# Kernel optimization log

Measured on AMD Instinct MI355X. Metric: run time of the kernel, lower is better.

Reference implementation:

```python
import jax, jax.numpy as jnp
import numpy as np

RC = 5.0
ATOM_TYPES = jnp.array([1, 6, 7, 8], dtype=jnp.int64)
L = 40.0   # cubic box edge; rc <= 0.5*L so the MIC branch of the torch module applies
N = 6000


def setup_inputs() -> dict:
    key = jax.random.key(0)
    k1, k2 = jax.random.split(key)
    coord = jax.random.uniform(k1, (N, 3), dtype=jnp.float32) * L
    cell = jnp.eye(3, dtype=jnp.float32) * L
    elems = jnp.array([1, 6, 7, 8])[jax.random.randint(k2, (N,), 0, 4)]
    return {"coord": coord, "cell": cell, "elems": elems}


def reference(coord, cell, elems):
    """JAX equivalent of PreprocessLayerTorch (MIC branch, rc <= min cell length / 2).

    The torch module emits a dynamic list of directed pairs ind_2 plus integer
    shifts; under jit we return the fixed-shape dense equivalent:
      - onehot:      (n, n_types) bool, AtomicOnehot of elems
      - dist_masked: (n, n) float, |r_j - r_i|_MIC where 0 < d < rc, else 0
      - shift:       (n, n, 3) int32 MIC lattice shifts
    ind_2 == nonzero(dist_masked > 0); same math, fixed shapes.
    """
    onehot = elems[:, None] == ATOM_TYPES[None, :]            # (n, n_types)

    h_inv = jnp.linalg.inv(cell)
    frac = coord @ h_inv                                      # (n, 3) fractional
    frac = frac - jnp.floor(frac)                             # wrap into [0,1)

    # dfrac[i, j] = frac_j - frac_i, minimum-image convention
    dfrac = frac[None, :, :] - frac[:, None, :]               # (n, n, 3)
    shift = -jnp.round(dfrac)                                 # (n, n, 3)
    dfrac = dfrac + shift
    d = dfrac @ cell                                          # (n, n, 3) Cartesian
    dist2 = jnp.sum(d * d, axis=-1)                           # (n, n)

    mask = (dist2 > 0.0) & (dist2 < RC * RC)
    dist = jnp.sqrt(jnp.where(mask, dist2, 1.0))              # safe sqrt
    dist_masked = jnp.where(mask, dist, 0.0)
    return onehot, dist_masked, shift.astype(jnp.int32)
```

## Files before the change

### kernel.cpp

```cpp
#include <hip/hip_runtime.h>
#include <math.h>

#define RC2 25.0f

typedef float f32x4 __attribute__((ext_vector_type(4)));

__global__ __launch_bounds__(256) void prep_kernel(
    const float* __restrict__ coord,
    const float* __restrict__ cell,
    const int* __restrict__ elems,
    float* __restrict__ onehot,
    float* __restrict__ frac,
    int n)
{
    int i = blockIdx.x * blockDim.x + threadIdx.x;
    if (i >= n) return;

    float a = cell[0], b = cell[1], c = cell[2];
    float d = cell[3], e = cell[4], f = cell[5];
    float g = cell[6], h = cell[7], k = cell[8];
    float A =  (e * k - f * h);
    float B = -(d * k - f * g);
    float C =  (d * h - e * g);
    float det = a * A + b * B + c * C;
    float inv = 1.0f / det;
    float m00 = A * inv,              m01 = -(b * k - c * h) * inv, m02 =  (b * f - c * e) * inv;
    float m10 = B * inv,              m11 =  (a * k - c * g) * inv, m12 = -(a * f - c * d) * inv;
    float m20 = C * inv,              m21 = -(a * h - b * g) * inv, m22 =  (a * e - b * d) * inv;

    float x = coord[i * 3 + 0];
    float y = coord[i * 3 + 1];
    float z = coord[i * 3 + 2];
    float fx = x * m00 + y * m10 + z * m20;
    float fy = x * m01 + y * m11 + z * m21;
    float fz = x * m02 + y * m12 + z * m22;
    fx -= floorf(fx); fy -= floorf(fy); fz -= floorf(fz);
    frac[i * 3 + 0] = fx;
    frac[i * 3 + 1] = fy;
    frac[i * 3 + 2] = fz;

    int el = elems[i];
    f32x4 oh;
    oh.x = (el == 1) ? 1.0f : 0.0f;
    oh.y = (el == 6) ? 1.0f : 0.0f;
    oh.z = (el == 7) ? 1.0f : 0.0f;
    oh.w = (el == 8) ? 1.0f : 0.0f;
    __builtin_nontemporal_store(oh, (f32x4*)(onehot + (size_t)i * 4));
}

__global__ __launch_bounds__(256) void pair_kernel(
    const float* __restrict__ frac,
    const float* __restrict__ cell,
    float* __restrict__ dist,
    float* __restrict__ shift,
    int n)
{
    __shared__ float sh_lds[1024 * 3];

    const int i  = blockIdx.y;
    const int J0 = blockIdx.x * 1024;
    const int t  = threadIdx.x;
    const int j0 = J0 + t * 4;

    if (j0 < n) {
        float c00 = cell[0], c01 = cell[1], c02 = cell[2];
        float c10 = cell[3], c11 = cell[4], c12 = cell[5];
        float c20 = cell[6], c21 = cell[7], c22 = cell[8];

        float fi0 = frac[i * 3 + 0];
        float fi1 = frac[i * 3 + 1];
        float fi2 = frac[i * 3 + 2];

        const float4* fj4 = (const float4*)(frac + (size_t)j0 * 3);
        float4 va = fj4[0], vb = fj4[1], vc = fj4[2];
        float fj[4][3] = {
            {va.x, va.y, va.z},
            {va.w, vb.x, vb.y},
            {vb.z, vb.w, vc.x},
            {vc.y, vc.z, vc.w}
        };

        f32x4 dout;
        float4 sh[3];
        float* shf = (float*)sh;

#pragma unroll
        for (int q = 0; q < 4; q++) {
            float d0 = fj[q][0] - fi0;
            float d1 = fj[q][1] - fi1;
            float d2 = fj[q][2] - fi2;
            float s0 = -rintf(d0);
            float s1 = -rintf(d1);
            float s2 = -rintf(d2);
            d0 += s0; d1 += s1; d2 += s2;
            float x = d0 * c00 + d1 * c10 + d2 * c20;
            float y = d0 * c01 + d1 * c11 + d2 * c21;
            float z = d0 * c02 + d1 * c12 + d2 * c22;
            float r2 = x * x + y * y + z * z;
            bool m = (r2 > 0.0f) && (r2 < RC2);
            dout[q] = m ? sqrtf(r2) : 0.0f;
            shf[q * 3 + 0] = s0;
            shf[q * 3 + 1] = s1;
            shf[q * 3 + 2] = s2;
        }

        __builtin_nontemporal_store(dout, (f32x4*)(dist + (size_t)i * n + j0));

        float4* lp = (float4*)(sh_lds + t * 12);
        lp[0] = sh[0];
        lp[1] = sh[1];
        lp[2] = sh[2];
    }

    __syncthreads();

    const int len = min(1024, n - J0);
    const int nf4 = (len * 3) >> 2;
    const f32x4* ls = (const f32x4*)sh_lds;
    f32x4* gp = (f32x4*)(shift + ((size_t)i * n + J0) * 3);
#pragma unroll
    for (int k = 0; k < 3; k++) {
        int q = k * 256 + t;
        if (q < nf4) __builtin_nontemporal_store(ls[q], gp + q);
    }
}

extern "C" void kernel_launch(void* const* d_in, const int* in_sizes, int n_in,
                              void* d_out, int out_size, void* d_ws, size_t ws_size,
                              hipStream_t stream)
{
    const float* coord = (const float*)d_in[0];
    const float* cell  = (const float*)d_in[1];
    const int*   elems = (const int*)d_in[2];
    int n = in_sizes[2];

    float* out    = (float*)d_out;
    float* onehot = out;
    float* dist   = out + (size_t)n * 4;
    float* shift  = out + (size_t)n * 4 + (size_t)n * n;

    float* frac = (float*)d_ws;

    dim3 b1(256);
    dim3 g1((n + 255) / 256);
    prep_kernel<<<g1, b1, 0, stream>>>(coord, cell, elems, onehot, frac, n);

    dim3 b2(256);
    dim3 g2((n + 1023) / 1024, n);
    pair_kernel<<<g2, b2, 0, stream>>>(frac, cell, dist, shift, n);
}
```

Baseline: 558.2 us.

## Use persistent grid-stride blocks and store shifts directly without LDS staging

```diff
diff --git a/kernel.cpp b/kernel.cpp
--- a/kernel.cpp
+++ b/kernel.cpp
@@ -53,19 +53,19 @@
     const float* __restrict__ cell,
     float* __restrict__ dist,
     float* __restrict__ shift,
-    int n)
+    int n, int nchunk, int total)
 {
-    __shared__ float sh_lds[1024 * 3];
+    const int t = threadIdx.x;
 
-    const int i  = blockIdx.y;
-    const int J0 = blockIdx.x * 1024;
-    const int t  = threadIdx.x;
-    const int j0 = J0 + t * 4;
+    float c00 = cell[0], c01 = cell[1], c02 = cell[2];
+    float c10 = cell[3], c11 = cell[4], c12 = cell[5];
+    float c20 = cell[6], c21 = cell[7], c22 = cell[8];
 
-    if (j0 < n) {
-        float c00 = cell[0], c01 = cell[1], c02 = cell[2];
-        float c10 = cell[3], c11 = cell[4], c12 = cell[5];
-        float c20 = cell[6], c21 = cell[7], c22 = cell[8];
+    for (int chunk = blockIdx.x; chunk < total; chunk += gridDim.x) {
+        int i  = chunk / nchunk;
+        int c  = chunk - i * nchunk;
+        int j0 = c * 1024 + t * 4;
+        if (j0 >= n) continue;
 
         float fi0 = frac[i * 3 + 0];
         float fi1 = frac[i * 3 + 1];
@@ -81,7 +81,7 @@
         };
 
         f32x4 dout;
-        float4 sh[3];
+        f32x4 sh[3];
         float* shf = (float*)sh;
 
 #pragma unroll
@@ -106,22 +106,10 @@
 
         __builtin_nontemporal_store(dout, (f32x4*)(dist + (size_t)i * n + j0));
 
-        float4* lp = (float4*)(sh_lds + t * 12);
-        lp[0] = sh[0];
-        lp[1] = sh[1];
-        lp[2] = sh[2];
-    }
-
-    __syncthreads();
-
-    const int len = min(1024, n - J0);
-    const int nf4 = (len * 3) >> 2;
-    const f32x4* ls = (const f32x4*)sh_lds;
-    f32x4* gp = (f32x4*)(shift + ((size_t)i * n + J0) * 3);
-#pragma unroll
-    for (int k = 0; k < 3; k++) {
-        int q = k * 256 + t;
-        if (q < nf4) __builtin_nontemporal_store(ls[q], gp + q);
+        f32x4* sp = (f32x4*)(shift + ((size_t)i * n + j0) * 3);
+        __builtin_nontemporal_store(sh[0], sp + 0);
+        __builtin_nontemporal_store(sh[1], sp + 1);
+        __builtin_nontemporal_store(sh[2], sp + 2);
     }
 }
 
@@ -145,7 +133,9 @@
     dim3 g1((n + 255) / 256);
     prep_kernel<<<g1, b1, 0, stream>>>(coord, cell, elems, onehot, frac, n);
 
+    int nchunk = (n + 1023) / 1024;
+    int total  = n * nchunk;
     dim3 b2(256);
-    dim3 g2((n + 1023) / 1024, n);
-    pair_kernel<<<g2, b2, 0, stream>>>(frac, cell, dist, shift, n);
+    dim3 g2(2048);
+    pair_kernel<<<g2, b2, 0, stream>>>(frac, cell, dist, shift, n, nchunk, total);
 }
```

After: 773.6 us. 1.39x slower.

## Use persistent grid-stride blocks for pair kernel and raw sqrt intrinsic

Applied to the files above, without the earlier changes.

```diff
diff --git a/kernel.cpp b/kernel.cpp
--- a/kernel.cpp
+++ b/kernel.cpp
@@ -53,75 +53,83 @@
     const float* __restrict__ cell,
     float* __restrict__ dist,
     float* __restrict__ shift,
-    int n)
+    int n, int nchunk, int total)
 {
     __shared__ float sh_lds[1024 * 3];
 
-    const int i  = blockIdx.y;
-    const int J0 = blockIdx.x * 1024;
-    const int t  = threadIdx.x;
-    const int j0 = J0 + t * 4;
+    const int t = threadIdx.x;
 
-    if (j0 < n) {
-        float c00 = cell[0], c01 = cell[1], c02 = cell[2];
-        float c10 = cell[3], c11 = cell[4], c12 = cell[5];
-        float c20 = cell[6], c21 = cell[7], c22 = cell[8];
+    float c00 = cell[0], c01 = cell[1], c02 = cell[2];
+    float c10 = cell[3], c11 = cell[4], c12 = cell[5];
+    float c20 = cell[6], c21 = cell[7], c22 = cell[8];
 
-        float fi0 = frac[i * 3 + 0];
-        float fi1 = frac[i * 3 + 1];
-        float fi2 = frac[i * 3 + 2];
+    for (int chunk = blockIdx.x; chunk < total; chunk += gridDim.x) {
+        int i  = chunk / nchunk;
+        int c  = chunk - i * nchunk;
+        int J0 = c * 1024;
+        int j0 = J0 + t * 4;
 
-        const float4* fj4 = (const float4*)(frac + (size_t)j0 * 3);
-        float4 va = fj4[0], vb = fj4[1], vc = fj4[2];
-        float fj[4][3] = {
-            {va.x, va.y, va.z},
-            {va.w, vb.x, vb.y},
-            {vb.z, vb.w, vc.x},
-            {vc.y, vc.z, vc.w}
-        };
+        if (j0 < n) {
+            float fi0 = frac[i * 3 + 0];
+            float fi1 = frac[i * 3 + 1];
+            float fi2 = frac[i * 3 + 2];
 
-        f32x4 dout;
-        float4 sh[3];
-        float* shf = (float*)sh;
+            const float4* fj4 = (const float4*)(frac + (size_t)j0 * 3);
+            float4 va = fj4[0], vb = fj4[1], vc = fj4[2];
+            float fj[4][3] = {
+                {va.x, va.y, va.z},
+                {va.w, vb.x, vb.y},
+                {vb.z, vb.w, vc.x},
+                {vc.y, vc.z, vc.w}
+            };
+
+            f32x4 dout;
+            f32x4 sh[3];
+            float* shf = (float*)sh;
 
 #pragma unroll
-        for (int q = 0; q < 4; q++) {
-            float d0 = fj[q][0] - fi0;
-            float d1 = fj[q][1] - fi1;
-            float d2 = fj[q][2] - fi2;
-            float s0 = -rintf(d0);
-            float s1 = -rintf(d1);
-            float s2 = -rintf(d2);
-            d0 += s0; d1 += s1; d2 += s2;
-            float x = d0 * c00 + d1 * c10 + d2 * c20;
-            float y = d0 * c01 + d1 * c11 + d2 * c21;
-            float z = d0 * c02 + d1 * c12 + d2 * c22;
-            float r2 = x * x + y * y + z * z;
-            bool m = (r2 > 0.0f) && (r2 < RC2);
-            dout[q] = m ? sqrtf(r2) : 0.0f;
-            shf[q * 3 + 0] = s0;
-            shf[q * 3 + 1] = s1;
-            shf[q * 3 + 2] = s2;
+            for (int q = 0; q < 4; q++) {
+                float e0 = fi0 - fj[q][0];
+                float e1 = fi1 - fj[q][1];
+                float e2 = fi2 - fj[q][2];
+                float s0 = rintf(e0);
+                float s1 = rintf(e1);
+                float s2 = rintf(e2);
+                float d0 = s0 - e0;
+                float d1 = s1 - e1;
+                float d2 = s2 - e2;
+                float x = d0 * c00 + d1 * c10 + d2 * c20;
+                float y = d0 * c01 + d1 * c11 + d2 * c21;
+                float z = d0 * c02 + d1 * c12 + d2 * c22;
+                float r2 = x * x + y * y + z * z;
+                bool m = (r2 > 0.0f) && (r2 < RC2);
+                dout[q] = m ? __builtin_amdgcn_sqrtf(r2) : 0.0f;
+                shf[q * 3 + 0] = s0;
+                shf[q * 3 + 1] = s1;
+                shf[q * 3 + 2] = s2;
+            }
+
+            __builtin_nontemporal_store(dout, (f32x4*)(dist + (size_t)i * n + j0));
+
+            f32x4* lp = (f32x4*)(sh_lds + t * 12);
+            lp[0] = sh[0];
+            lp[1] = sh[1];
+            lp[2] = sh[2];
         }
 
-        __builtin_nontemporal_store(dout, (f32x4*)(dist + (size_t)i * n + j0));
+        __syncthreads();
 
-        float4* lp = (float4*)(sh_lds + t * 12);
-        lp[0] = sh[0];
-        lp[1] = sh[1];
-        lp[2] = sh[2];
-    }
+        const int len = min(1024, n - J0);
+        const int nf4 = (len * 3) >> 2;
+        const f32x4* ls = (const f32x4*)sh_lds;
+        f32x4* gp = (f32x4*)(shift + ((size_t)i * n + J0) * 3);
+#pragma unroll
+        for (int k = 0; k < 3; k++) {
+            int q = k * 256 + t;
+            if (q < nf4) __builtin_nontemporal_store(ls[q], gp + q);
+        }
 
-    __syncthreads();
-
-    const int len = min(1024, n - J0);
-    const int nf4 = (len * 3) >> 2;
-    const f32x4* ls = (const f32x4*)sh_lds;
-    f32x4* gp = (f32x4*)(shift + ((size_t)i * n + J0) * 3);
-#pragma unroll
-    for (int k = 0; k < 3; k++) {
-        int q = k * 256 + t;
-        if (q < nf4) __builtin_nontemporal_store(ls[q], gp + q);
+        __syncthreads();
     }
 }
 
@@ -145,7 +153,9 @@
     dim3 g1((n + 255) / 256);
     prep_kernel<<<g1, b1, 0, stream>>>(coord, cell, elems, onehot, frac, n);
 
+    int nchunk = (n + 1023) / 1024;
+    int total  = n * nchunk;
     dim3 b2(256);
-    dim3 g2((n + 1023) / 1024, n);
-    pair_kernel<<<g2, b2, 0, stream>>>(frac, cell, dist, shift, n);
+    dim3 g2(2000);
+    pair_kernel<<<g2, b2, 0, stream>>>(frac, cell, dist, shift, n, nchunk, total);
 }
```

New measurement: 568.9 us. About the same (+1.9%).
